# Kernel optimization log

Hardware: AMD Instinct MI355X
Metric: run time of the kernel (lower is better)

Reference implementation:

```python
import jax, jax.numpy as jnp
from jax import lax
import numpy as np

B, N, M, K, NS, C = 8, 8192, 512, 6, 16, 13  # batch, points, clusters, nc2p, nsample, classes
D = 64  # point feature dim

def _fps(xyz, m):
    """Furthest point sampling over one cloud [n,3] -> [m] int32 indices."""
    n = xyz.shape[0]
    def body(carry, _):
        dist, last = carry
        d = jnp.sum((xyz - xyz[last]) ** 2, axis=-1)
        dist = jnp.minimum(dist, d)
        return (dist, jnp.argmax(dist).astype(jnp.int32)), last
    (_, _), idxs = lax.scan(body, (jnp.full((n,), 1e10, xyz.dtype), jnp.int32(0)), None, length=m)
    return idxs

def _gather(src, idx):
    # src [B, S, d] (or [B, S]), idx [B, ...] -> [B, ..., d]
    return jax.vmap(lambda s, i: s[i])(src, idx)

def _scatter_weighted(idx, w, val, m):
    # idx [B,n,K] cluster ids, w [B,n,K] weights, val [B,n,d] -> weighted mean per cluster [B,m,d]
    def one(i_b, w_b, v_b):
        num = jnp.zeros((m, v_b.shape[-1]), v_b.dtype).at[i_b].add(w_b[..., None] * v_b[:, None, :])
        den = jnp.zeros((m,), w_b.dtype).at[i_b].add(w_b)
        return num / jnp.maximum(den, 1e-8)[:, None]
    return jax.vmap(one)(idx, w, val)

def _mlp2(x, W1, W2):
    return jax.nn.relu(jax.nn.relu(x @ W1) @ W2)

def _forward(pointcloud, clouds_knn, onehot_label, label,
             bb_Wk1, bb_Wk2, bb_Wg, head_W1, head_W2,
             slic_Wf1, slic_Wf2, slic_Wx1, slic_Wx2, slic_Wm1, slic_Wm2):
    xyz = pointcloud[..., :3]              # [B,N,3]
    fea = pointcloud[..., 3:]              # [B,N,3]
    # --- FPS + KNN cluster association (pointops.furthestsampling / knnquerycluster) ---
    cluster_idx = jax.vmap(lambda x: _fps(x, M))(xyz)            # [B,M]
    cluster_xyz = _gather(xyz, cluster_idx)                      # [B,M,3]
    d2 = jnp.sum((xyz[:, :, None, :] - cluster_xyz[:, None, :, :]) ** 2, axis=-1)  # [B,N,M]
    _, c2p_idx_abs = lax.top_k(-d2, K)                           # [B,N,K] cluster ids
    c2p_idx = _gather(cluster_idx, c2p_idx_abs)                  # [B,N,K] point ids of clusters
    # --- association matrix + per-cluster label histogram (pointops.assomatrixpluslabel) ---
    def build(i_b, lab_b):
        A = jnp.zeros((M, N), jnp.float32).at[i_b, jnp.arange(N)[:, None]].add(1.0)
        L = jnp.zeros((M, C), jnp.float32).at[i_b.reshape(-1), jnp.repeat(lab_b, K)].add(1.0)
        return A, A.sum(-1, keepdims=True), L
    asso_matrix, sp_nei_cnt, sp_lab = jax.vmap(build)(c2p_idx_abs, label)
    # --- backbone (LPE_stn): per-point local KNN branch (max-pool) + global feature branch ---
    hk = jnp.max(_mlp2(clouds_knn, bb_Wk1, bb_Wk2), axis=2)      # [B,N,64]
    hg = jax.nn.relu(fea @ bb_Wg)                                # [B,N,64]
    p_fea = hk + hg                                              # [B,N,64]
    out = jax.nn.relu(p_fea @ head_W1) @ head_W2                 # [B,N,C] semantic logits
    # --- init_fea: average associated point features per cluster ---
    sp_fea = jnp.einsum('bmn,bnd->bmd', asso_matrix, p_fea) / jnp.maximum(sp_nei_cnt, 1.0)
    sp_xyz = cluster_xyz
    fea_dist = None
    for l in range(4):
        fd = _gather(sp_fea, c2p_idx_abs) - p_fea[:, :, None, :]   # [B,N,K,64]
        xd = _gather(sp_xyz, c2p_idx_abs) - xyz[:, :, None, :]     # [B,N,K,3]
        wf = _mlp2(fd, slic_Wf1[l], slic_Wf2[l])                   # [B,N,K,16]
        wx = _mlp2(xd, slic_Wx1[l], slic_Wx2[l])                   # [B,N,K,16]
        pm = _mlp2(p_fea, slic_Wm1[l], slic_Wm2[l])                # [B,N,16]
        logits = jnp.sum(wf * wx * pm[:, :, None, :], axis=-1)    # [B,N,K]
        w = jax.nn.softmax(logits, axis=-1)
        sp_fea = _scatter_weighted(c2p_idx_abs, w, p_fea, M)
        sp_xyz = _scatter_weighted(c2p_idx_abs, w, xyz, M)
        fea_dist = w
    final_asso = fea_dist                                         # [B,N,K]
    # --- reconstruction branch ---
    p2sp_idx = jnp.argmax(final_asso, axis=2)                     # [B,N]
    sel = jnp.take_along_axis(c2p_idx_abs, p2sp_idx[..., None], 2)[..., 0]
    re_p_xyz = _gather(sp_xyz, sel)                               # [B,N,3]
    sp_label = _scatter_weighted(c2p_idx_abs, final_asso, onehot_label, M)  # [B,M,C]
    c2p_label = _gather(sp_label, c2p_idx_abs)                    # [B,N,K,C]
    re_p_label = jnp.sum(c2p_label * final_asso[..., None], axis=2)  # [B,N,C]
    sp_pseudo_lab = jnp.argmax(sp_lab, axis=2)                    # [B,M]
    sp_pseudo_lab_onehot = jax.nn.one_hot(sp_pseudo_lab, C, dtype=jnp.float32).transpose(0, 2, 1)
    return (final_asso, cluster_idx, c2p_idx, c2p_idx_abs, out, re_p_xyz, re_p_label,
            fea_dist, p_fea, sp_label.transpose(0, 2, 1), sp_pseudo_lab, sp_pseudo_lab_onehot)

def setup_inputs() -> dict:
    key = jax.random.key(0)
    ks = jax.random.split(key, 20)
    s = lambda k, shp, sc: (jax.random.normal(k, shp, jnp.float32) * sc)
    return {
        'pointcloud': jax.random.normal(ks[0], (B, N, 6), jnp.float32),
        'clouds_knn': jax.random.normal(ks[1], (B, N, NS, 2), jnp.float32),
        'onehot_label': jax.random.uniform(ks[2], (B, N, C), jnp.float32),
        'label': jax.random.randint(ks[3], (B, N), 0, C, jnp.int32),
        'bb_Wk1': s(ks[4], (2, 32), 0.5), 'bb_Wk2': s(ks[5], (32, D), 0.15),
        'bb_Wg': s(ks[6], (3, D), 0.4),
        'head_W1': s(ks[7], (D, D), 0.12), 'head_W2': s(ks[8], (D, C), 0.12),
        'slic_Wf1': s(ks[9], (4, D, 16), 0.12), 'slic_Wf2': s(ks[10], (4, 16, 16), 0.25),
        'slic_Wx1': s(ks[11], (4, 3, 16), 0.5), 'slic_Wx2': s(ks[12], (4, 16, 16), 0.25),
        'slic_Wm1': s(ks[13], (4, D, 16), 0.12), 'slic_Wm2': s(ks[14], (4, 16, 16), 0.25),
    }

def reference(pointcloud, clouds_knn, onehot_label, label,
              bb_Wk1, bb_Wk2, bb_Wg, head_W1, head_W2,
              slic_Wf1, slic_Wf2, slic_Wx1, slic_Wx2, slic_Wm1, slic_Wm2):
    return _forward(pointcloud, clouds_knn, onehot_label, label,
                    bb_Wk1, bb_Wk2, bb_Wg, head_W1, head_W2,
                    slic_Wf1, slic_Wf2, slic_Wx1, slic_Wx2, slic_Wm1, slic_Wm2)
```

## Files before the change

### kernel.cpp

```cpp
#include <hip/hip_runtime.h>

#define BB 8
#define NN 8192
#define MM 512
#define KK 6
#define NSAMP 16
#define CC 13
#define DD 64

#define O_ASSO   0u
#define O_CIDX   393216u
#define O_C2P    397312u
#define O_C2PA   790528u
#define O_OUT    1183744u
#define O_RPXYZ  2035712u
#define O_RPLAB  2232320u
#define O_FDIST  3084288u
#define O_PFEA   3477504u
#define O_SPLABT 7671808u
#define O_PSLAB  7725056u
#define O_PSOH   7729152u

__device__ __forceinline__ unsigned long long dpp_max_u64(unsigned long long k) {
  int lo = (int)(unsigned)(k & 0xFFFFFFFFull);
  int hi = (int)(unsigned)(k >> 32);
#define DPP_STEP(ctrl)                                                         \
  {                                                                            \
    int nlo = __builtin_amdgcn_update_dpp(0, lo, ctrl, 0xf, 0xf, true);        \
    int nhi = __builtin_amdgcn_update_dpp(0, hi, ctrl, 0xf, 0xf, true);        \
    unsigned long long nk =                                                    \
        ((unsigned long long)(unsigned)nhi << 32) | (unsigned)nlo;             \
    unsigned long long ck =                                                    \
        ((unsigned long long)(unsigned)hi << 32) | (unsigned)lo;               \
    if (nk > ck) { lo = nlo; hi = nhi; }                                       \
  }
  DPP_STEP(0x111)
  DPP_STEP(0x112)
  DPP_STEP(0x114)
  DPP_STEP(0x118)
  DPP_STEP(0x142)
  DPP_STEP(0x143)
#undef DPP_STEP
  return ((unsigned long long)(unsigned)hi << 32) | (unsigned)lo;
}

__global__ __launch_bounds__(512, 1) void k_fps(const float* __restrict__ pc,
                                                int* __restrict__ cidx,
                                                float* __restrict__ cxyz,
                                                float* __restrict__ out) {
  __shared__ float sx[NN], sy[NN], sz[NN];
  __shared__ unsigned long long s_best[2][8];
  const int t = threadIdx.x;
  const int b = blockIdx.x;
  const float* xb = pc + (size_t)b * NN * 6;
  float px[16], py[16], pz[16], dist[16];
#pragma unroll
  for (int j = 0; j < 16; ++j) {
    int p = t + j * 512;
    float X = xb[(size_t)p*6+0], Y = xb[(size_t)p*6+1], Z = xb[(size_t)p*6+2];
    px[j] = X; py[j] = Y; pz[j] = Z; dist[j] = 1e10f;
    sx[p] = X; sy[p] = Y; sz[p] = Z;
  }
  __syncthreads();
  float lx = sx[0], ly = sy[0], lz = sz[0];
  if (t == 0) {
    cidx[b*MM] = 0; out[O_CIDX + b*MM] = 0.0f;
    cxyz[(size_t)b*MM*3+0] = lx; cxyz[(size_t)b*MM*3+1] = ly; cxyz[(size_t)b*MM*3+2] = lz;
  }
  const int lane = t & 63, wave = t >> 6;
  for (int step = 1; step < MM; ++step) {
    float bv = -1.0f; int bp = 0;
#pragma unroll
    for (int j = 0; j < 16; ++j) {
      float dx = px[j]-lx, dy = py[j]-ly, dz = pz[j]-lz;
      float d = __fadd_rn(__fadd_rn(__fmul_rn(dx,dx), __fmul_rn(dy,dy)), __fmul_rn(dz,dz));
      float nd = fminf(dist[j], d);
      dist[j] = nd;
      if (nd > bv) { bv = nd; bp = t + j*512; }
    }
    unsigned long long key = ((unsigned long long)__float_as_uint(bv) << 32)
                           | (unsigned)(0xFFFFFFFFu - (unsigned)bp);
    key = dpp_max_u64(key);
    if (lane == 63) s_best[step & 1][wave] = key;
    __syncthreads();
    const ulonglong2* sb = (const ulonglong2*)s_best[step & 1];
    ulonglong2 q0 = sb[0], q1 = sb[1], q2 = sb[2], q3 = sb[3];
    unsigned long long kk = q0.x;
    if (q0.y > kk) kk = q0.y;
    if (q1.x > kk) kk = q1.x;
    if (q1.y > kk) kk = q1.y;
    if (q2.x > kk) kk = q2.x;
    if (q2.y > kk) kk = q2.y;
    if (q3.x > kk) kk = q3.x;
    if (q3.y > kk) kk = q3.y;
    int p = (int)(0xFFFFFFFFu - (unsigned)(kk & 0xFFFFFFFFull));
    lx = sx[p]; ly = sy[p]; lz = sz[p];
    if (t == 0) {
      cidx[b*MM + step] = p;
      out[O_CIDX + b*MM + step] = (float)p;
      cxyz[((size_t)b*MM + step)*3+0] = lx;
      cxyz[((size_t)b*MM + step)*3+1] = ly;
      cxyz[((size_t)b*MM + step)*3+2] = lz;
    }
  }
}

__attribute__((amdgpu_waves_per_eu(1, 2)))
__global__ __launch_bounds__(256) void k_pfea(const float* __restrict__ pc,
                                              const float* __restrict__ knn,
                                              const float* __restrict__ Wk1,
                                              const float* __restrict__ Wk2,
                                              const float* __restrict__ Wg,
                                              const float* __restrict__ hW1,
                                              const float* __restrict__ hW2,
                                              float* __restrict__ xyz,
                                              float* __restrict__ out) {
  int i = blockIdx.x * 256 + threadIdx.x;
  const float2* pr = (const float2*)(pc + (size_t)i*6);
  float2 r0 = pr[0], r1 = pr[1], r2 = pr[2];
  float* xo = xyz + (size_t)i*3;
  xo[0] = r0.x; xo[1] = r0.y; xo[2] = r1.x;
  float acc[DD];
#pragma unroll
  for (int d = 0; d < DD; ++d) acc[d] = -3.4e38f;
  const float* kp = knn + (size_t)i * NSAMP * 2;
  for (int s = 0; s < NSAMP; ++s) {
    float u = kp[s*2+0], v2 = kp[s*2+1];
    float h1[32];
#pragma unroll
    for (int j = 0; j < 32; ++j) h1[j] = fmaxf(u*Wk1[j] + v2*Wk1[32+j], 0.f);
#pragma unroll
    for (int d = 0; d < DD; ++d) {
      float tt = 0.f;
#pragma unroll
      for (int j = 0; j < 32; ++j) tt += h1[j]*Wk2[j*DD+d];
      acc[d] = fmaxf(acc[d], tt);
    }
  }
  float f0 = r1.y, f1 = r2.x, f2 = r2.y;
#pragma unroll
  for (int d = 0; d < DD; ++d) {
    float hg = fmaxf(f0*Wg[d] + f1*Wg[DD+d] + f2*Wg[2*DD+d], 0.f);
    acc[d] = fmaxf(acc[d], 0.f) + hg;
    out[O_PFEA + (size_t)i*DD + d] = acc[d];
  }
  float o[CC];
#pragma unroll
  for (int c = 0; c < CC; ++c) o[c] = 0.f;
  for (int d = 0; d < DD; ++d) {
    float t1 = 0.f;
#pragma unroll
    for (int j = 0; j < DD; ++j) t1 += acc[j]*hW1[j*DD+d];
    t1 = fmaxf(t1, 0.f);
#pragma unroll
    for (int c = 0; c < CC; ++c) o[c] += t1*hW2[d*CC+c];
  }
#pragma unroll
  for (int c = 0; c < CC; ++c) out[O_OUT + (size_t)i*CC + c] = o[c];
}

__global__ __launch_bounds__(256) void k_knn(const float* __restrict__ xyz,
                      const float* __restrict__ cxyz,
                      const int* __restrict__ cidx, int* __restrict__ c2p,
                      float* __restrict__ out) {
  __shared__ float4 sc[MM];
  int i = blockIdx.x * 256 + threadIdx.x;
  int b = i >> 13;
  for (int m = threadIdx.x; m < MM; m += 256) {
    sc[m] = make_float4(cxyz[((size_t)b*MM+m)*3+0], cxyz[((size_t)b*MM+m)*3+1],
                        cxyz[((size_t)b*MM+m)*3+2], 0.f);
  }
  __syncthreads();
  float x = xyz[(size_t)i*3+0], y = xyz[(size_t)i*3+1], z = xyz[(size_t)i*3+2];
  float dv[KK]; int di[KK];
#pragma unroll
  for (int j = 0; j < KK; ++j) { dv[j] = 3.4e38f; di[j] = 0; }
  for (int m = 0; m < MM; ++m) {
    float4 c = sc[m];
    float dx = x - c.x, dy = y - c.y, dz = z - c.z;
    float d = __fadd_rn(__fadd_rn(__fmul_rn(dx,dx), __fmul_rn(dy,dy)), __fmul_rn(dz,dz));
    if (d < dv[KK-1]) {
      float v = d; int vi = m; bool ins = false;
#pragma unroll
      for (int j = 0; j < KK; ++j) {
        bool doit = ins || (v < dv[j]);
        float tv = doit ? dv[j] : v; int ti = doit ? di[j] : vi;
        if (doit) { dv[j] = v; di[j] = vi; }
        v = tv; vi = ti; ins = doit;
      }
    }
  }
#pragma unroll
  for (int k = 0; k < KK; ++k) {
    c2p[(size_t)i*KK+k] = di[k];
    out[O_C2PA + (size_t)i*KK + k] = (float)di[k];
    out[O_C2P  + (size_t)i*KK + k] = (float)cidx[b*MM + di[k]];
  }
}

__global__ void k_count(const int* __restrict__ c2p, const int* __restrict__ label,
                        int* __restrict__ cnt, int* __restrict__ labcnt) {
  int i = blockIdx.x*256 + threadIdx.x;
  int b = i >> 13;
  int lab = label[i];
#pragma unroll
  for (int k = 0; k < KK; ++k) {
    int m = c2p[(size_t)i*KK+k];
    atomicAdd(&cnt[b*MM+m], 1);
    atomicAdd(&labcnt[(b*MM+m)*CC + lab], 1);
  }
}

__global__ void k_scan(const int* __restrict__ cnt, int* __restrict__ offs, int* __restrict__ cursor) {
  __shared__ int s[MM];
  int b = blockIdx.x, t = threadIdx.x;
  s[t] = cnt[b*MM+t];
  __syncthreads();
  for (int off = 1; off < MM; off <<= 1) {
    int v = 0;
    if (t >= off) v = s[t-off];
    __syncthreads();
    if (t >= off) s[t] += v;
    __syncthreads();
  }
  int ex = (t == 0) ? 0 : s[t-1];
  offs[b*MM+t] = ex;
  cursor[b*MM+t] = ex;
}

__global__ void k_fill(const int* __restrict__ c2p, int* __restrict__ cursor, int* __restrict__ entries) {
  int i = blockIdx.x*256 + threadIdx.x;
  int b = i >> 13;
  int nloc = i & (NN-1);
#pragma unroll
  for (int k = 0; k < KK; ++k) {
    int m = c2p[(size_t)i*KK+k];
    int pos = atomicAdd(&cursor[b*MM+m], 1);
    entries[(size_t)b*NN*KK + pos] = nloc*KK + k;
  }
}

__global__ void k_pseudo(const int* __restrict__ labcnt, float* __restrict__ out) {
  int bm = blockIdx.x*256 + threadIdx.x;
  int b = bm >> 9, m = bm & (MM-1);
  int best = 0, bv = labcnt[bm*CC];
#pragma unroll
  for (int c = 1; c < CC; ++c) { int v = labcnt[bm*CC+c]; if (v > bv) { bv = v; best = c; } }
  out[O_PSLAB + bm] = (float)best;
#pragma unroll
  for (int c = 0; c < CC; ++c)
    out[O_PSOH + ((size_t)b*CC + c)*MM + m] = (c == best) ? 1.0f : 0.0f;
}

__global__ __launch_bounds__(256, 1) void k_scat(const float* __restrict__ pfea,
                          const float* __restrict__ xyz,
                          const float* __restrict__ w,
                          const float* __restrict__ cxyz,
                          const float* __restrict__ onehot,
                          const int* __restrict__ entries, const int* __restrict__ offs,
                          const int* __restrict__ cnt,
                          const float* __restrict__ Wf1n,
                          float* __restrict__ sp_fea, float* __restrict__ sp_xyz,
                          float* __restrict__ sp_label, float* __restrict__ smeta,
                          float* __restrict__ out) {
  int bm = blockIdx.x;
  int b = bm >> 9, m = bm & (MM-1);
  int t = threadIdx.x;
  int wv = t >> 6, lane = t & 63;
  int base = b*NN*KK;
  int st = offs[bm], n_e = cnt[bm];
  __shared__ int   s_ent[1024];
  __shared__ float s_w[1024];
  __shared__ float s_f[4][DD], s_x[4][4], s_l[4][16], s_d[4];
  __shared__ float s_sf[DD], s_part[16][17];
  float acc = 0.f, accx = 0.f, accl = 0.f, den = 0.f;
  for (int c0 = 0; c0 < n_e; c0 += 1024) {
    int cn = min(1024, n_e - c0);
    __syncthreads();
    for (int e = t; e < cn; e += 256) {
      int ee = entries[base + st + c0 + e];
      s_ent[e] = ee;
      s_w[e] = w ? w[(size_t)base + ee] : 1.0f;
    }
    __syncthreads();
    for (int e = wv; e < cn; e += 4) {
      int ee = s_ent[e]; float ww = s_w[e];
      int n = ee / KK;
      acc += ww * pfea[((size_t)b*NN+n)*DD + lane];
      if (lane < 3) accx += ww * xyz[((size_t)b*NN+n)*3 + lane];
      if (onehot && lane < CC) accl += ww * onehot[((size_t)b*NN+n)*CC + lane];
      den += ww;
    }
  }
  s_f[wv][lane] = acc;
  if (lane < 4)  s_x[wv][lane] = (lane < 3) ? accx : 0.f;
  if (lane < 16) s_l[wv][lane] = (lane < CC) ? accl : 0.f;
  if (lane == 0) s_d[wv] = den;
  __syncthreads();
  if (wv == 0) {
    float A  = s_f[0][lane] + s_f[1][lane] + s_f[2][lane] + s_f[3][lane];
    float Dn = s_d[0] + s_d[1] + s_d[2] + s_d[3];
    float dv = w ? fmaxf(Dn, 1e-8f) : fmaxf(Dn, 1.0f);
    float sfv = A / dv;
    sp_fea[(size_t)bm*DD + lane] = sfv;
    s_sf[lane] = sfv;
    if (lane < 3) {
      float X = w ? (s_x[0][lane]+s_x[1][lane]+s_x[2][lane]+s_x[3][lane]) / dv
                  : cxyz[bm*3+lane];
      sp_xyz[bm*3+lane] = X;
      if (Wf1n) smeta[bm*20 + 16 + lane] = X;
    }
    if (onehot && lane < CC) {
      float L = (s_l[0][lane]+s_l[1][lane]+s_l[2][lane]+s_l[3][lane]) / fmaxf(Dn, 1e-8f);
      sp_label[(size_t)bm*CC + lane] = L;
      out[O_SPLABT + ((size_t)b*CC + lane)*MM + m] = L;
    }
  }
  if (Wf1n) {
    __syncthreads();
    int c = t & 15, part = t >> 4;
    float pr = 0.f;
#pragma unroll
    for (int q = 0; q < 4; ++q)
      pr += s_sf[part*4+q] * Wf1n[(part*4+q)*16 + c];
    s_part[part][c] = pr;
    __syncthreads();
    if (t < 16) {
      float sm = 0.f;
#pragma unroll
      for (int q = 0; q < 16; ++q) sm += s_part[q][t];
      smeta[bm*20 + t] = sm;
    }
  }
}

__attribute__((amdgpu_waves_per_eu(1, 2)))
__global__ __launch_bounds__(256) void k_slicw(const float* __restrict__ pfea,
                        const float* __restrict__ xyz,
                        const float* __restrict__ smeta,
                        const int* __restrict__ c2p,
                        const float* __restrict__ Wf1, const float* __restrict__ Wf2,
                        const float* __restrict__ Wx1, const float* __restrict__ Wx2,
                        const float* __restrict__ Wm1, const float* __restrict__ Wm2,
                        float* __restrict__ wout, float* __restrict__ wout2) {
  int i = blockIdx.x*256 + threadIdx.x;
  int b = i >> 13;
  float pf[DD];
  const float4* pf4 = (const float4*)(pfea + (size_t)i*DD);
#pragma unroll
  for (int q = 0; q < DD/4; ++q) {
    float4 t = pf4[q];
    pf[q*4+0] = t.x; pf[q*4+1] = t.y; pf[q*4+2] = t.z; pf[q*4+3] = t.w;
  }
  float a[16];
#pragma unroll
  for (int c = 0; c < 16; ++c) a[c] = 0.f;
#pragma unroll
  for (int d = 0; d < DD; ++d) {
    float f = pf[d];
#pragma unroll
    for (int c = 0; c < 16; ++c) a[c] += f*Wm1[d*16+c];
  }
  float pm[16];
#pragma unroll
  for (int c2 = 0; c2 < 16; ++c2) {
    float t = 0.f;
#pragma unroll
    for (int c = 0; c < 16; ++c) t += fmaxf(a[c], 0.f)*Wm2[c*16+c2];
    pm[c2] = fmaxf(t, 0.f);
  }
  float pfd[16];
#pragma unroll
  for (int c = 0; c < 16; ++c) pfd[c] = 0.f;
#pragma unroll
  for (int d = 0; d < DD; ++d) {
    float f = pf[d];
#pragma unroll
    for (int c = 0; c < 16; ++c) pfd[c] += f*Wf1[d*16+c];
  }
  float x = xyz[(size_t)i*3+0], y = xyz[(size_t)i*3+1], z = xyz[(size_t)i*3+2];
  float lg[KK];
#pragma unroll 1
  for (int k = 0; k < KK; ++k) {
    int m = c2p[(size_t)i*KK+k];
    int bm = (b << 9) + m;
    const float4* mp = (const float4*)(smeta + (size_t)bm*20);
    float4 m0 = mp[0], m1 = mp[1], m2 = mp[2], m3 = mp[3], m4 = mp[4];
    float wa[16];
    wa[0]=m0.x-pfd[0];  wa[1]=m0.y-pfd[1];  wa[2]=m0.z-pfd[2];  wa[3]=m0.w-pfd[3];
    wa[4]=m1.x-pfd[4];  wa[5]=m1.y-pfd[5];  wa[6]=m1.z-pfd[6];  wa[7]=m1.w-pfd[7];
    wa[8]=m2.x-pfd[8];  wa[9]=m2.y-pfd[9];  wa[10]=m2.z-pfd[10]; wa[11]=m2.w-pfd[11];
    wa[12]=m3.x-pfd[12]; wa[13]=m3.y-pfd[13]; wa[14]=m3.z-pfd[14]; wa[15]=m3.w-pfd[15];
    float wf[16];
#pragma unroll
    for (int c2 = 0; c2 < 16; ++c2) {
      float t = 0.f;
#pragma unroll
      for (int c = 0; c < 16; ++c) t += fmaxf(wa[c], 0.f)*Wf2[c*16+c2];
      wf[c2] = fmaxf(t, 0.f);
    }
    float dx = m4.x - x, dy = m4.y - y, dz = m4.z - z;
    float ax[16];
#pragma unroll
    for (int c = 0; c < 16; ++c)
      ax[c] = fmaxf(dx*Wx1[c] + dy*Wx1[16+c] + dz*Wx1[32+c], 0.f);
    float lgk = 0.f;
#pragma unroll
    for (int c2 = 0; c2 < 16; ++c2) {
      float t = 0.f;
#pragma unroll
      for (int c = 0; c < 16; ++c) t += ax[c]*Wx2[c*16+c2];
      lgk += fmaxf(t, 0.f)*wf[c2]*pm[c2];
    }
    lg[k] = lgk;
  }
  float mx = lg[0];
#pragma unroll
  for (int k = 1; k < KK; ++k) mx = fmaxf(mx, lg[k]);
  float e[KK], s = 0.f;
#pragma unroll
  for (int k = 0; k < KK; ++k) { e[k] = expf(lg[k]-mx); s += e[k]; }
#pragma unroll
  for (int k = 0; k < KK; ++k) {
    float wv = e[k]/s;
    wout[(size_t)i*KK+k] = wv;
    if (wout2) wout2[(size_t)i*KK+k] = wv;
  }
}

__global__ __launch_bounds__(256) void k_final(const float* __restrict__ sp_xyz, const float* __restrict__ sp_label,
                        const int* __restrict__ c2p, float* __restrict__ out) {
  int i = blockIdx.x*256 + threadIdx.x;
  int b = i >> 13;
  float w[KK]; int id[KK];
#pragma unroll
  for (int k = 0; k < KK; ++k) {
    w[k] = out[O_ASSO + (size_t)i*KK+k];
    id[k] = c2p[(size_t)i*KK+k];
  }
  int best = 0; float bv = w[0];
#pragma unroll
  for (int k = 1; k < KK; ++k) if (w[k] > bv) { bv = w[k]; best = k; }
  int sel = id[best];
#pragma unroll
  for (int c = 0; c < 3; ++c)
    out[O_RPXYZ + (size_t)i*3+c] = sp_xyz[((size_t)b*MM+sel)*3+c];
  float acc[CC];
#pragma unroll
  for (int c = 0; c < CC; ++c) acc[c] = 0.f;
#pragma unroll
  for (int k = 0; k < KK; ++k) {
    const float* sl = sp_label + ((size_t)b*MM + id[k])*CC;
    float ww = w[k];
#pragma unroll
    for (int c = 0; c < CC; ++c) acc[c] += ww*sl[c];
  }
#pragma unroll
  for (int c = 0; c < CC; ++c) out[O_RPLAB + (size_t)i*CC+c] = acc[c];
}

extern "C" void kernel_launch(void* const* d_in, const int* in_sizes, int n_in,
                              void* d_out, int out_size, void* d_ws, size_t ws_size,
                              hipStream_t stream) {
  const float* pc     = (const float*)d_in[0];
  const float* knn    = (const float*)d_in[1];
  const float* onehot = (const float*)d_in[2];
  const int*   label  = (const int*)d_in[3];
  const float* Wk1    = (const float*)d_in[4];
  const float* Wk2    = (const float*)d_in[5];
  const float* Wg     = (const float*)d_in[6];
  const float* hW1    = (const float*)d_in[7];
  const float* hW2    = (const float*)d_in[8];
  const float* Wf1    = (const float*)d_in[9];
  const float* Wf2    = (const float*)d_in[10];
  const float* Wx1    = (const float*)d_in[11];
  const float* Wx2    = (const float*)d_in[12];
  const float* Wm1    = (const float*)d_in[13];
  const float* Wm2    = (const float*)d_in[14];
  float* out = (float*)d_out;

  float* wsf = (float*)d_ws;
  size_t o = 0;
  float* xyz     = wsf + o; o += (size_t)BB*NN*3;
  float* cxyz    = wsf + o; o += (size_t)BB*MM*3;
  int*   cidx    = (int*)(wsf + o); o += BB*MM;
  int*   c2p     = (int*)(wsf + o); o += (size_t)BB*NN*KK;
  int*   cnt     = (int*)(wsf + o); o += BB*MM;
  int*   labcnt  = (int*)(wsf + o); o += BB*MM*CC;
  int*   offs    = (int*)(wsf + o); o += BB*MM;
  int*   cursor  = (int*)(wsf + o); o += BB*MM;
  int*   entries = (int*)(wsf + o); o += (size_t)BB*NN*KK;
  float* sp_fea  = wsf + o; o += (size_t)BB*MM*DD;
  float* sp_xyz  = wsf + o; o += (size_t)BB*MM*3;
  float* sp_label= wsf + o; o += (size_t)BB*MM*CC;
  float* smeta   = wsf + o; o += (size_t)BB*MM*20;

  hipMemsetAsync(cnt, 0, (size_t)(BB*MM + BB*MM*CC)*sizeof(int), stream);

  k_fps  <<<BB, 512, 0, stream>>>(pc, cidx, cxyz, out);
  k_pfea <<<BB*NN/256, 256, 0, stream>>>(pc, knn, Wk1, Wk2, Wg, hW1, hW2, xyz, out);
  k_knn  <<<BB*NN/256, 256, 0, stream>>>(xyz, cxyz, cidx, c2p, out);
  k_count<<<BB*NN/256, 256, 0, stream>>>(c2p, label, cnt, labcnt);
  k_scan <<<BB, MM, 0, stream>>>(cnt, offs, cursor);
  k_fill <<<BB*NN/256, 256, 0, stream>>>(c2p, cursor, entries);
  k_pseudo<<<BB*MM/256, 256, 0, stream>>>(labcnt, out);
  k_scat<<<BB*MM, 256, 0, stream>>>(out + O_PFEA, xyz, nullptr, cxyz, nullptr,
      entries, offs, cnt, Wf1 , sp_fea, sp_xyz, nullptr, smeta, out);
  for (int l = 0; l < 4; ++l) {
    k_slicw<<<BB*NN/256, 256, 0, stream>>>(out + O_PFEA, xyz, smeta, c2p,
        Wf1 + l*DD*16, Wf2 + l*256, Wx1 + l*48, Wx2 + l*256,
        Wm1 + l*DD*16, Wm2 + l*256,
        out + O_ASSO, (l == 3) ? (out + O_FDIST) : nullptr);
    k_scat<<<BB*MM, 256, 0, stream>>>(out + O_PFEA, xyz, out + O_ASSO, cxyz,
        (l == 3) ? onehot : nullptr, entries, offs, cnt,
        (l < 3) ? (Wf1 + (l+1)*DD*16) : nullptr,
        sp_fea, sp_xyz, sp_label, smeta, out);
  }
  k_final<<<BB*NN/256, 256, 0, stream>>>(sp_xyz, sp_label, c2p, out);
}
```

Before: 1.621 ms.

## Fuse cluster count, scan, fill and pseudo-label into one per-batch LDS kernel

Replaces four kernels (global-atomic count, scan, fill, pseudo-label) and a memset with a single per-batch kernel. It does the histogram, prefix scan, argmax and CSR fill using shared-memory atomics. FPS also buffers its selected indices and coordinates in shared memory and writes them out once at the end, so the per-step global stores from thread 0 leave the serial loop. The cost is that the CSR stage now runs on only 8 blocks, which cuts parallelism, and entry order within a cluster can still vary from run to run.

```diff
diff --git a/kernel.cpp b/kernel.cpp
--- a/kernel.cpp
+++ b/kernel.cpp
@@ -50,6 +50,8 @@
                                                 float* __restrict__ out) {
   __shared__ float sx[NN], sy[NN], sz[NN];
   __shared__ unsigned long long s_best[2][8];
+  __shared__ int   s_pidx[MM];
+  __shared__ float s_px[MM], s_py[MM], s_pz[MM];
   const int t = threadIdx.x;
   const int b = blockIdx.x;
   const float* xb = pc + (size_t)b * NN * 6;
@@ -63,10 +65,7 @@
   }
   __syncthreads();
   float lx = sx[0], ly = sy[0], lz = sz[0];
-  if (t == 0) {
-    cidx[b*MM] = 0; out[O_CIDX + b*MM] = 0.0f;
-    cxyz[(size_t)b*MM*3+0] = lx; cxyz[(size_t)b*MM*3+1] = ly; cxyz[(size_t)b*MM*3+2] = lz;
-  }
+  if (t == 0) { s_pidx[0] = 0; s_px[0] = lx; s_py[0] = ly; s_pz[0] = lz; }
   const int lane = t & 63, wave = t >> 6;
   for (int step = 1; step < MM; ++step) {
     float bv = -1.0f; int bp = 0;
@@ -96,12 +95,18 @@
     int p = (int)(0xFFFFFFFFu - (unsigned)(kk & 0xFFFFFFFFull));
     lx = sx[p]; ly = sy[p]; lz = sz[p];
     if (t == 0) {
-      cidx[b*MM + step] = p;
-      out[O_CIDX + b*MM + step] = (float)p;
-      cxyz[((size_t)b*MM + step)*3+0] = lx;
-      cxyz[((size_t)b*MM + step)*3+1] = ly;
-      cxyz[((size_t)b*MM + step)*3+2] = lz;
-    }
+      s_pidx[step] = p;
+      s_px[step] = lx; s_py[step] = ly; s_pz[step] = lz;
+    }
+  }
+  __syncthreads();
+  if (t < MM) {
+    int p = s_pidx[t];
+    cidx[b*MM + t] = p;
+    out[O_CIDX + b*MM + t] = (float)p;
+    cxyz[((size_t)b*MM + t)*3+0] = s_px[t];
+    cxyz[((size_t)b*MM + t)*3+1] = s_py[t];
+    cxyz[((size_t)b*MM + t)*3+2] = s_pz[t];
   }
 }
 
@@ -198,58 +203,63 @@
   }
 }
 
-__global__ void k_count(const int* __restrict__ c2p, const int* __restrict__ label,
-                        int* __restrict__ cnt, int* __restrict__ labcnt) {
-  int i = blockIdx.x*256 + threadIdx.x;
-  int b = i >> 13;
-  int lab = label[i];
-#pragma unroll
-  for (int k = 0; k < KK; ++k) {
-    int m = c2p[(size_t)i*KK+k];
-    atomicAdd(&cnt[b*MM+m], 1);
-    atomicAdd(&labcnt[(b*MM+m)*CC + lab], 1);
-  }
-}
-
-__global__ void k_scan(const int* __restrict__ cnt, int* __restrict__ offs, int* __restrict__ cursor) {
-  __shared__ int s[MM];
+__global__ __launch_bounds__(1024) void k_csr(const int* __restrict__ c2p,
+                                              const int* __restrict__ label,
+                                              int* __restrict__ cnt_g,
+                                              int* __restrict__ offs_g,
+                                              int* __restrict__ entries,
+                                              float* __restrict__ out) {
+  __shared__ int s_cnt[MM];
+  __shared__ int s_off[MM];
+  __shared__ int s_cur[MM];
+  __shared__ int s_lab[MM*CC];
   int b = blockIdx.x, t = threadIdx.x;
-  s[t] = cnt[b*MM+t];
+  for (int i = t; i < MM; i += 1024) s_cnt[i] = 0;
+  for (int i = t; i < MM*CC; i += 1024) s_lab[i] = 0;
+  __syncthreads();
+  const int* cb = c2p + (size_t)b*NN*KK;
+  const int* lb = label + (size_t)b*NN;
+  for (int n = t; n < NN; n += 1024) {
+    int lab = lb[n];
+#pragma unroll
+    for (int k = 0; k < KK; ++k) {
+      int m = cb[(size_t)n*KK+k];
+      atomicAdd(&s_cnt[m], 1);
+      atomicAdd(&s_lab[m*CC+lab], 1);
+    }
+  }
+  __syncthreads();
+  if (t < MM) s_off[t] = s_cnt[t];
   __syncthreads();
   for (int off = 1; off < MM; off <<= 1) {
     int v = 0;
-    if (t >= off) v = s[t-off];
-    __syncthreads();
-    if (t >= off) s[t] += v;
-    __syncthreads();
-  }
-  int ex = (t == 0) ? 0 : s[t-1];
-  offs[b*MM+t] = ex;
-  cursor[b*MM+t] = ex;
-}
-
-__global__ void k_fill(const int* __restrict__ c2p, int* __restrict__ cursor, int* __restrict__ entries) {
-  int i = blockIdx.x*256 + threadIdx.x;
-  int b = i >> 13;
-  int nloc = i & (NN-1);
-#pragma unroll
-  for (int k = 0; k < KK; ++k) {
-    int m = c2p[(size_t)i*KK+k];
-    int pos = atomicAdd(&cursor[b*MM+m], 1);
-    entries[(size_t)b*NN*KK + pos] = nloc*KK + k;
-  }
-}
-
-__global__ void k_pseudo(const int* __restrict__ labcnt, float* __restrict__ out) {
-  int bm = blockIdx.x*256 + threadIdx.x;
-  int b = bm >> 9, m = bm & (MM-1);
-  int best = 0, bv = labcnt[bm*CC];
-#pragma unroll
-  for (int c = 1; c < CC; ++c) { int v = labcnt[bm*CC+c]; if (v > bv) { bv = v; best = c; } }
-  out[O_PSLAB + bm] = (float)best;
-#pragma unroll
-  for (int c = 0; c < CC; ++c)
-    out[O_PSOH + ((size_t)b*CC + c)*MM + m] = (c == best) ? 1.0f : 0.0f;
+    if (t < MM && t >= off) v = s_off[t-off];
+    __syncthreads();
+    if (t < MM && t >= off) s_off[t] += v;
+    __syncthreads();
+  }
+  if (t < MM) {
+    int ex = (t == 0) ? 0 : s_off[t-1];
+    s_cur[t] = ex;
+    offs_g[b*MM+t] = ex;
+    cnt_g[b*MM+t] = s_cnt[t];
+    int best = 0, bv = s_lab[t*CC];
+#pragma unroll
+    for (int c = 1; c < CC; ++c) { int v = s_lab[t*CC+c]; if (v > bv) { bv = v; best = c; } }
+    out[O_PSLAB + b*MM + t] = (float)best;
+#pragma unroll
+    for (int c = 0; c < CC; ++c)
+      out[O_PSOH + ((size_t)b*CC + c)*MM + t] = (c == best) ? 1.0f : 0.0f;
+  }
+  __syncthreads();
+  for (int n = t; n < NN; n += 1024) {
+#pragma unroll
+    for (int k = 0; k < KK; ++k) {
+      int m = cb[(size_t)n*KK+k];
+      int pos = atomicAdd(&s_cur[m], 1);
+      entries[(size_t)b*NN*KK + pos] = n*KK + k;
+    }
+  }
 }
 
 __global__ __launch_bounds__(256, 1) void k_scat(const float* __restrict__ pfea,
@@ -486,24 +496,17 @@
   int*   cidx    = (int*)(wsf + o); o += BB*MM;
   int*   c2p     = (int*)(wsf + o); o += (size_t)BB*NN*KK;
   int*   cnt     = (int*)(wsf + o); o += BB*MM;
-  int*   labcnt  = (int*)(wsf + o); o += BB*MM*CC;
   int*   offs    = (int*)(wsf + o); o += BB*MM;
-  int*   cursor  = (int*)(wsf + o); o += BB*MM;
   int*   entries = (int*)(wsf + o); o += (size_t)BB*NN*KK;
   float* sp_fea  = wsf + o; o += (size_t)BB*MM*DD;
   float* sp_xyz  = wsf + o; o += (size_t)BB*MM*3;
   float* sp_label= wsf + o; o += (size_t)BB*MM*CC;
   float* smeta   = wsf + o; o += (size_t)BB*MM*20;
 
-  hipMemsetAsync(cnt, 0, (size_t)(BB*MM + BB*MM*CC)*sizeof(int), stream);
-
   k_fps  <<<BB, 512, 0, stream>>>(pc, cidx, cxyz, out);
   k_pfea <<<BB*NN/256, 256, 0, stream>>>(pc, knn, Wk1, Wk2, Wg, hW1, hW2, xyz, out);
   k_knn  <<<BB*NN/256, 256, 0, stream>>>(xyz, cxyz, cidx, c2p, out);
-  k_count<<<BB*NN/256, 256, 0, stream>>>(c2p, label, cnt, labcnt);
-  k_scan <<<BB, MM, 0, stream>>>(cnt, offs, cursor);
-  k_fill <<<BB*NN/256, 256, 0, stream>>>(c2p, cursor, entries);
-  k_pseudo<<<BB*MM/256, 256, 0, stream>>>(labcnt, out);
+  k_csr  <<<BB, 1024, 0, stream>>>(c2p, label, cnt, offs, entries, out);
   k_scat<<<BB*MM, 256, 0, stream>>>(out + O_PFEA, xyz, nullptr, cxyz, nullptr,
       entries, offs, cnt, Wf1 , sp_fea, sp_xyz, nullptr, smeta, out);
   for (int l = 0; l < 4; ++l) {
```

After: 1.570 ms. 1.03x faster.
